# Kernel tuning notes

Hardware: AMD Instinct MI355X
Metric: run time of the kernel (lower is better)

## Reference

```python
import jax, jax.numpy as jnp
import numpy as np

N = 100_000      # nodes
E = 3_200_000    # edges (avg degree 32)
F = 16           # irrep feature channels
IR = 4           # (max_l+1)**2 with max_l = 1
DENOM = 32.0     # denominator init kwarg
EPS = 1e-9
INV_S3 = 1.0 / np.sqrt(3.0).astype(np.float32)  # CG norm for 1x1->0
INV_S2 = 1.0 / np.sqrt(2.0).astype(np.float32)  # CG norm for 1x1->1


def setup_inputs() -> dict:
    key = jax.random.key(0)
    k0, k1, k2, k3, k4 = jax.random.split(key, 5)
    positions = jax.random.normal(k0, (N, 3), jnp.float32)
    node_feats = jax.random.normal(k1, (N, F, IR), jnp.float32)
    W = jax.random.normal(k2, (IR, IR), jnp.float32) / np.float32(np.sqrt(IR))
    b = jnp.zeros((IR,), jnp.float32)
    senders = jax.random.randint(k3, (E,), 0, N)
    receivers = jax.random.randint(k4, (E,), 0, N)
    return dict(positions=positions, node_feats=node_feats, W=W, b=b,
                senders=senders, receivers=receivers)


def reference(positions, node_feats, W, b, senders, receivers):
    # --- edge update: SH of normalized relative position, CG tensor product ---
    d = positions[receivers] - positions[senders]               # [E, 3]
    d = d / (jnp.linalg.norm(d, axis=-1, keepdims=True) + EPS)  # unit direction
    # real spherical harmonics up to l=1: sh0 = 1, sh1 = unit direction
    sh1 = d[:, None, :]                                         # [E, 1, 3]

    x = node_feats[senders]                                     # [E, F, 4]
    x0 = x[..., 0:1]                                            # l=0 part [E,F,1]
    x1 = x[..., 1:4]                                            # l=1 part [E,F,3]

    # CG paths with l3 <= max_l = 1:
    #   0x0->0 (identity), 1x1->0 (dot / sqrt3)
    out0 = x0 + jnp.sum(x1 * sh1, axis=-1, keepdims=True) * INV_S3      # [E,F,1]
    #   0x1->1, 1x0->1 (identities), 1x1->1 (cross / sqrt2)
    cross = jnp.cross(x1, jnp.broadcast_to(sh1, x1.shape))
    out1 = x0 * sh1 + x1 + cross * INV_S2                               # [E,F,3]
    tp = jnp.concatenate([out0, out1], axis=-1)                         # [E,F,4]

    # --- node update: segment-sum over receivers, scale, Dense over coeff dim ---
    agg = jax.ops.segment_sum(tp, receivers, num_segments=positions.shape[0])
    agg = agg / DENOM                                                   # [N,F,4]
    return agg @ W + b                                                  # [N,F,4]
```

## Files before the change

kernel.cpp:

```cpp
#include <hip/hip_runtime.h>


#define F_DIM 16
#define BIN_SHIFT 5
#define BIN_NODES (1 << BIN_SHIFT)
#define CHUNK 4096
#define STG (CHUNK / 256)
#define CAP_LDS 1408
#define MAXBINS 4096

__global__ void __launch_bounds__(256) init_kernel(int* __restrict__ binCur,
                                                   int nbins, int cap)
{
    int b = blockIdx.x * blockDim.x + threadIdx.x;
    if (b < nbins) binCur[b] = b * cap;
}

__global__ void __launch_bounds__(256) pos_pack_kernel(
    const float* __restrict__ pos, float4* __restrict__ posf4, int N)
{
    int n = blockIdx.x * blockDim.x + threadIdx.x;
    if (n >= N) return;
    posf4[n] = make_float4(pos[3*n], pos[3*n+1], pos[3*n+2], 0.f);
}

__global__ void __launch_bounds__(256) build_bins_kernel(
    const int* __restrict__ senders, const int* __restrict__ receivers,
    int* __restrict__ binCur, int* __restrict__ bins,
    int nbins, int cap, int E)
{
    __shared__ int hist[MAXBINS];
    int t = threadIdx.x;
    for (int i = t; i < nbins; i += 256) hist[i] = 0;
    __syncthreads();

    int base = blockIdx.x * CHUNK;
    unsigned pk[STG], br[STG];
#pragma unroll
    for (int k = 0; k < STG; ++k) {
        int e = base + k * 256 + t;
        if (e < E) {
            int r = receivers[e];
            int s = senders[e];
            int bb = r >> BIN_SHIFT;
            int rank = atomicAdd(&hist[bb], 1);
            pk[k] = ((unsigned)s << BIN_SHIFT) | (unsigned)(r & (BIN_NODES - 1));
            br[k] = ((unsigned)bb << 13) | (unsigned)rank;
        } else {
            br[k] = 0xFFFFFFFFu;
        }
    }
    __syncthreads();

    for (int i = t; i < nbins; i += 256) {
        int c = hist[i];
        if (c > 0) hist[i] = atomicAdd(&binCur[i], c);
    }
    __syncthreads();

#pragma unroll
    for (int k = 0; k < STG; ++k) {
        if (br[k] == 0xFFFFFFFFu) continue;
        int bb   = (int)(br[k] >> 13);
        int rank = (int)(br[k] & 8191u);
        int dest = hist[bb] + rank;
        if (dest < (bb + 1) * cap)
            bins[dest] = (int)pk[k];
    }
}

__device__ __forceinline__ void edge_acc_d(
    float dx, float dy, float dz, const float4& fx,
    float& a0, float& a1, float& a2, float& a3)
{
    const float INV_S3 = 0.5773502691896258f;
    const float INV_S2 = 0.7071067811865476f;
    float dot = fx.y*dx + fx.z*dy + fx.w*dz;
    a0 += fx.x + dot * INV_S3;
    float c0 = fx.z*dz - fx.w*dy;
    float c1 = fx.w*dx - fx.y*dz;
    float c2 = fx.y*dy - fx.z*dx;
    a1 += fx.x*dx + fx.y + c0 * INV_S2;
    a2 += fx.x*dy + fx.z + c1 * INV_S2;
    a3 += fx.x*dz + fx.w + c2 * INV_S2;
}

__global__ void __launch_bounds__(256) bin_gather_kernel(
    const float4* __restrict__ posf4,
    const float* __restrict__ nf,
    const int* __restrict__ bins,
    const int* __restrict__ binCur,
    const float* __restrict__ W,
    const float* __restrict__ Bias,
    float* __restrict__ out,
    int N, int cap)
{
    __shared__ int   lcsr[CAP_LDS];
    __shared__ float ldx[CAP_LDS];
    __shared__ float ldy[CAP_LDS];
    __shared__ float ldz[CAP_LDS];
    __shared__ int lhist[BIN_NODES];
    __shared__ int lscan[BIN_NODES];
    __shared__ int lstart[BIN_NODES];

    int t = threadIdx.x;
    int bin = blockIdx.x;
    int node0 = bin << BIN_SHIFT;
    int gbase = bin * cap;

    int cnt = binCur[bin] - gbase;
    if (cnt > cap) cnt = cap;

    if (t < BIN_NODES) lhist[t] = 0;
    __syncthreads();

    for (int j = t; j < cnt; j += 256)
        atomicAdd(&lhist[((unsigned)bins[gbase + j]) & (BIN_NODES - 1)], 1);
    __syncthreads();

    if (t < BIN_NODES) lscan[t] = lhist[t];
    __syncthreads();
    for (int off = 1; off < BIN_NODES; off <<= 1) {
        int v = (t < BIN_NODES && t >= off) ? lscan[t - off] : 0;
        __syncthreads();
        if (t < BIN_NODES) lscan[t] += v;
        __syncthreads();
    }
    if (t < BIN_NODES) { lstart[t] = lscan[t] - lhist[t]; lhist[t] = 0; }
    __syncthreads();

    for (int j = t; j < cnt; j += 256) {
        unsigned pk = (unsigned)bins[gbase + j];
        int rl = (int)(pk & (BIN_NODES - 1));
        int s  = (int)(pk >> BIN_SHIFT);
        int rank = atomicAdd(&lhist[rl], 1);
        int dest = lstart[rl] + rank;
        lcsr[dest] = s;
        float4 ps = posf4[s];
        float4 pr = posf4[node0 + rl];
        float dx = pr.x - ps.x;
        float dy = pr.y - ps.y;
        float dz = pr.z - ps.z;
        float d2 = dx*dx + dy*dy + dz*dz;
        float inv = __builtin_amdgcn_rsqf(fmaxf(d2, 1e-18f));
        ldx[dest] = dx * inv;
        ldy[dest] = dy * inv;
        ldz[dest] = dz * inv;
    }
    __syncthreads();

    float w[16];
#pragma unroll
    for (int i = 0; i < 16; ++i) w[i] = W[i];
    float b0 = Bias[0], b1 = Bias[1], b2 = Bias[2], b3 = Bias[3];
    const float sc = 1.0f / 32.0f;

    int f = t & 15;
    const float4* nf4 = (const float4*)nf;

    for (int nl = t >> 4; nl < BIN_NODES; nl += 16) {
        int n = node0 + nl;
        if (n >= N) break;
        int s0 = lstart[nl];
        int dcnt = lscan[nl] - s0;

        float a0 = 0.f, a1 = 0.f, a2 = 0.f, a3 = 0.f;
        int j = 0;
        for (; j + 4 <= dcnt; j += 4) {
            int s_0 = lcsr[s0 + j + 0];
            int s_1 = lcsr[s0 + j + 1];
            int s_2 = lcsr[s0 + j + 2];
            int s_3 = lcsr[s0 + j + 3];
            float4 q0 = nf4[(unsigned)(s_0 * F_DIM + f)];
            float4 q1 = nf4[(unsigned)(s_1 * F_DIM + f)];
            float4 q2 = nf4[(unsigned)(s_2 * F_DIM + f)];
            float4 q3 = nf4[(unsigned)(s_3 * F_DIM + f)];
            float x0 = ldx[s0 + j + 0], y0 = ldy[s0 + j + 0], z0 = ldz[s0 + j + 0];
            float x1 = ldx[s0 + j + 1], y1 = ldy[s0 + j + 1], z1 = ldz[s0 + j + 1];
            float x2 = ldx[s0 + j + 2], y2 = ldy[s0 + j + 2], z2 = ldz[s0 + j + 2];
            float x3 = ldx[s0 + j + 3], y3 = ldy[s0 + j + 3], z3 = ldz[s0 + j + 3];
            edge_acc_d(x0, y0, z0, q0, a0, a1, a2, a3);
            edge_acc_d(x1, y1, z1, q1, a0, a1, a2, a3);
            edge_acc_d(x2, y2, z2, q2, a0, a1, a2, a3);
            edge_acc_d(x3, y3, z3, q3, a0, a1, a2, a3);
        }
        for (; j < dcnt; ++j) {
            int s = lcsr[s0 + j];
            float4 q = nf4[(unsigned)(s * F_DIM + f)];
            edge_acc_d(ldx[s0 + j], ldy[s0 + j], ldz[s0 + j], q, a0, a1, a2, a3);
        }

        a0 *= sc; a1 *= sc; a2 *= sc; a3 *= sc;
        float4 o;
        o.x = a0*w[0] + a1*w[4] + a2*w[8]  + a3*w[12] + b0;
        o.y = a0*w[1] + a1*w[5] + a2*w[9]  + a3*w[13] + b1;
        o.z = a0*w[2] + a1*w[6] + a2*w[10] + a3*w[14] + b2;
        o.w = a0*w[3] + a1*w[7] + a2*w[11] + a3*w[15] + b3;
        ((float4*)out)[(size_t)n * F_DIM + f] = o;
    }
}

__global__ void __launch_bounds__(256) hist_kernel(
    const int* __restrict__ receivers, int* __restrict__ deg,
    int* __restrict__ rank, int E)
{
    int e = blockIdx.x * blockDim.x + threadIdx.x;
    if (e >= E) return;
    rank[e] = atomicAdd(&deg[receivers[e]], 1);
}

__global__ void __launch_bounds__(256) alloc_kernel(
    const int* __restrict__ deg, int* __restrict__ start,
    int* __restrict__ cursor, int N)
{
    __shared__ int tmp[256];
    __shared__ int base;
    int t = threadIdx.x;
    int n = blockIdx.x * blockDim.x + t;
    int v = (n < N) ? deg[n] : 0;
    tmp[t] = v;
    __syncthreads();
    for (int off = 1; off < 256; off <<= 1) {
        int x = (t >= off) ? tmp[t - off] : 0;
        __syncthreads();
        tmp[t] += x;
        __syncthreads();
    }
    int incl = tmp[t];
    if (t == 255) base = atomicAdd(cursor, incl);
    __syncthreads();
    if (n < N) start[n] = base + incl - v;
}

__global__ void __launch_bounds__(256) scatter_kernel(
    const int* __restrict__ senders, const int* __restrict__ receivers,
    const int* __restrict__ rank, const int* __restrict__ start,
    int* __restrict__ csr_s, int E)
{
    int e = blockIdx.x * blockDim.x + threadIdx.x;
    if (e >= E) return;
    csr_s[start[receivers[e]] + rank[e]] = senders[e];
}

__global__ void __launch_bounds__(256) gather_kernel(
    const float* __restrict__ pos,
    const float* __restrict__ nf,
    const int* __restrict__ csr_s,
    const int* __restrict__ start,
    const int* __restrict__ deg,
    const float* __restrict__ W,
    const float* __restrict__ b,
    float* __restrict__ out,
    int N)
{
    const float INV_S3 = 0.5773502691896258f;
    const float INV_S2 = 0.7071067811865476f;

    int tid = blockIdx.x * blockDim.x + threadIdx.x;
    int n = tid >> 4;
    if (n >= N) return;
    int f = tid & 15;

    float rx = pos[3*n], ry = pos[3*n+1], rz = pos[3*n+2];
    int s0 = start[n];
    int dcnt = deg[n];
    float a0 = 0.f, a1 = 0.f, a2 = 0.f, a3 = 0.f;
    const float4* nf4 = (const float4*)nf;

    int s = (dcnt > 0) ? csr_s[s0] : 0;
    for (int j = 0; j < dcnt; ++j) {
        int s_next = (j + 1 < dcnt) ? csr_s[s0 + j + 1] : 0;
        float dx = rx - pos[3*s], dy = ry - pos[3*s+1], dz = rz - pos[3*s+2];
        float d2 = dx*dx + dy*dy + dz*dz;
        float inv = __builtin_amdgcn_rsqf(fmaxf(d2, 1e-18f));
        dx *= inv; dy *= inv; dz *= inv;
        float4 x = nf4[(unsigned)(s * F_DIM + f)];
        float x0 = x.x, x1 = x.y, x2 = x.z, x3 = x.w;
        float dot = x1*dx + x2*dy + x3*dz;
        a0 += x0 + dot * INV_S3;
        float c0 = x2*dz - x3*dy, c1 = x3*dx - x1*dz, c2 = x1*dy - x2*dx;
        a1 += x0*dx + x1 + c0 * INV_S2;
        a2 += x0*dy + x2 + c1 * INV_S2;
        a3 += x0*dz + x3 + c2 * INV_S2;
        s = s_next;
    }
    const float sc = 1.0f / 32.0f;
    a0 *= sc; a1 *= sc; a2 *= sc; a3 *= sc;
    float4 o;
    o.x = a0*W[0] + a1*W[4] + a2*W[8]  + a3*W[12] + b[0];
    o.y = a0*W[1] + a1*W[5] + a2*W[9]  + a3*W[13] + b[1];
    o.z = a0*W[2] + a1*W[6] + a2*W[10] + a3*W[14] + b[2];
    o.w = a0*W[3] + a1*W[7] + a2*W[11] + a3*W[15] + b[3];
    ((float4*)out)[tid] = o;
}

extern "C" void kernel_launch(void* const* d_in, const int* in_sizes, int n_in,
                              void* d_out, int out_size, void* d_ws, size_t ws_size,
                              hipStream_t stream)
{
    const float* pos       = (const float*)d_in[0];
    const float* nf        = (const float*)d_in[1];
    const float* W         = (const float*)d_in[2];
    const float* b         = (const float*)d_in[3];
    const int*   senders   = (const int*)d_in[4];
    const int*   receivers = (const int*)d_in[5];

    int N = in_sizes[0] / 3;
    int E = in_sizes[4];
    float* out = (float*)d_out;
    const int blk = 256;

    int nbins = (N + BIN_NODES - 1) >> BIN_SHIFT;
    int cap   = E / nbins + 384;
    size_t need = ((size_t)N * 4 + (size_t)nbins * cap + nbins) * sizeof(float);

    if (nbins <= MAXBINS && cap <= CAP_LDS && ws_size >= need) {
        float4* posf4 = (float4*)d_ws;
        int* binCur = (int*)(posf4 + N);
        int* bins   = binCur + nbins;

        pos_pack_kernel<<<(N + blk - 1) / blk, blk, 0, stream>>>(pos, posf4, N);
        init_kernel<<<(nbins + blk - 1) / blk, blk, 0, stream>>>(binCur, nbins, cap);
        build_bins_kernel<<<(E + CHUNK - 1) / CHUNK, blk, 0, stream>>>(
            senders, receivers, binCur, bins, nbins, cap, E);
        bin_gather_kernel<<<nbins, blk, 0, stream>>>(
            posf4, nf, bins, binCur, W, b, out, N, cap);
    } else {
        int* cursor = (int*)d_ws;
        int* deg    = cursor + 1;
        int* start  = deg + N;
        int* rank   = start + N;
        int* csr_s  = rank + E;

        hipMemsetAsync(cursor, 0, (size_t)(1 + N) * sizeof(int), stream);
        hist_kernel<<<(E + blk - 1) / blk, blk, 0, stream>>>(receivers, deg, rank, E);
        alloc_kernel<<<(N + blk - 1) / blk, blk, 0, stream>>>(deg, start, cursor, N);
        scatter_kernel<<<(E + blk - 1) / blk, blk, 0, stream>>>(
            senders, receivers, rank, start, csr_s, E);
        long total = (long)N * F_DIM;
        gather_kernel<<<(unsigned)((total + blk - 1) / blk), blk, 0, stream>>>(
            pos, nf, csr_s, start, deg, W, b, out, N);
    }
}
```

Baseline: 287.5 us.

## Use 64-node bins split across two gather blocks with packed float4 edge records

Bins double to 64 nodes, which halves the number of global bin cursors and the atomics on them. The bin-building kernel moves to 512 threads and 8192-edge chunks and reads receivers twice instead of holding per-edge state in registers. Each bin is now processed by two gather blocks, each filtering the edges for its 32-node half, so every block reads the whole bin. Edge direction and sender index are packed into one float4 in LDS so each edge needs a single LDS load, and a guard for LDS overflow is added.

```diff
diff --git a/kernel.cpp b/kernel.cpp
--- a/kernel.cpp
+++ b/kernel.cpp
@@ -2,12 +2,12 @@
 
 
 #define F_DIM 16
-#define BIN_SHIFT 5
+#define BIN_SHIFT 6
 #define BIN_NODES (1 << BIN_SHIFT)
-#define CHUNK 4096
-#define STG (CHUNK / 256)
+#define HALF_NODES (BIN_NODES / 2)
+#define CHUNK 8192
 #define CAP_LDS 1408
-#define MAXBINS 4096
+#define MAXBINS 2048
 
 __global__ void __launch_bounds__(256) init_kernel(int* __restrict__ binCur,
                                                    int nbins, int cap)
@@ -24,48 +24,38 @@
     posf4[n] = make_float4(pos[3*n], pos[3*n+1], pos[3*n+2], 0.f);
 }
 
-__global__ void __launch_bounds__(256) build_bins_kernel(
+__global__ void __launch_bounds__(512) build_bins_kernel(
     const int* __restrict__ senders, const int* __restrict__ receivers,
     int* __restrict__ binCur, int* __restrict__ bins,
     int nbins, int cap, int E)
 {
-    __shared__ int hist[MAXBINS];
+    __shared__ int hbase[MAXBINS];
+    __shared__ int hrank[MAXBINS];
     int t = threadIdx.x;
-    for (int i = t; i < nbins; i += 256) hist[i] = 0;
+    for (int i = t; i < nbins; i += 512) { hbase[i] = 0; hrank[i] = 0; }
     __syncthreads();
 
     int base = blockIdx.x * CHUNK;
-    unsigned pk[STG], br[STG];
-#pragma unroll
-    for (int k = 0; k < STG; ++k) {
-        int e = base + k * 256 + t;
-        if (e < E) {
-            int r = receivers[e];
-            int s = senders[e];
-            int bb = r >> BIN_SHIFT;
-            int rank = atomicAdd(&hist[bb], 1);
-            pk[k] = ((unsigned)s << BIN_SHIFT) | (unsigned)(r & (BIN_NODES - 1));
-            br[k] = ((unsigned)bb << 13) | (unsigned)rank;
-        } else {
-            br[k] = 0xFFFFFFFFu;
-        }
-    }
-    __syncthreads();
-
-    for (int i = t; i < nbins; i += 256) {
-        int c = hist[i];
-        if (c > 0) hist[i] = atomicAdd(&binCur[i], c);
-    }
-    __syncthreads();
-
-#pragma unroll
-    for (int k = 0; k < STG; ++k) {
-        if (br[k] == 0xFFFFFFFFu) continue;
-        int bb   = (int)(br[k] >> 13);
-        int rank = (int)(br[k] & 8191u);
-        int dest = hist[bb] + rank;
+    int end  = base + CHUNK; if (end > E) end = E;
+
+    for (int e = base + t; e < end; e += 512)
+        atomicAdd(&hbase[((unsigned)receivers[e]) >> BIN_SHIFT], 1);
+    __syncthreads();
+
+    for (int i = t; i < nbins; i += 512) {
+        int c = hbase[i];
+        hbase[i] = (c > 0) ? atomicAdd(&binCur[i], c) : 0;
+    }
+    __syncthreads();
+
+    for (int e = base + t; e < end; e += 512) {
+        int r = receivers[e];
+        int s = senders[e];
+        int bb = r >> BIN_SHIFT;
+        int rank = atomicAdd(&hrank[bb], 1);
+        int dest = hbase[bb] + rank;
         if (dest < (bb + 1) * cap)
-            bins[dest] = (int)pk[k];
+            bins[dest] = (s << BIN_SHIFT) | (r & (BIN_NODES - 1));
     }
 }
 
@@ -95,57 +85,62 @@
     float* __restrict__ out,
     int N, int cap)
 {
-    __shared__ int   lcsr[CAP_LDS];
-    __shared__ float ldx[CAP_LDS];
-    __shared__ float ldy[CAP_LDS];
-    __shared__ float ldz[CAP_LDS];
-    __shared__ int lhist[BIN_NODES];
-    __shared__ int lscan[BIN_NODES];
-    __shared__ int lstart[BIN_NODES];
+    __shared__ float4 ledge[CAP_LDS];
+    __shared__ int lhist[HALF_NODES];
+    __shared__ int lscan[HALF_NODES];
+    __shared__ int lstart[HALF_NODES];
 
     int t = threadIdx.x;
-    int bin = blockIdx.x;
-    int node0 = bin << BIN_SHIFT;
+    int bin  = blockIdx.x >> 1;
+    int half = blockIdx.x & 1;
+    int node0 = (bin << BIN_SHIFT) + half * HALF_NODES;
     int gbase = bin * cap;
 
     int cnt = binCur[bin] - gbase;
     if (cnt > cap) cnt = cap;
 
-    if (t < BIN_NODES) lhist[t] = 0;
-    __syncthreads();
-
-    for (int j = t; j < cnt; j += 256)
-        atomicAdd(&lhist[((unsigned)bins[gbase + j]) & (BIN_NODES - 1)], 1);
-    __syncthreads();
-
-    if (t < BIN_NODES) lscan[t] = lhist[t];
-    __syncthreads();
-    for (int off = 1; off < BIN_NODES; off <<= 1) {
-        int v = (t < BIN_NODES && t >= off) ? lscan[t - off] : 0;
+    if (t < HALF_NODES) lhist[t] = 0;
+    __syncthreads();
+
+    for (int j = t; j < cnt; j += 256) {
+        int rl = bins[gbase + j] & (BIN_NODES - 1);
+        if ((rl >> 5) == half) atomicAdd(&lhist[rl & (HALF_NODES - 1)], 1);
+    }
+    __syncthreads();
+
+    if (t < HALF_NODES) lscan[t] = lhist[t];
+    __syncthreads();
+    for (int off = 1; off < HALF_NODES; off <<= 1) {
+        int v = (t < HALF_NODES && t >= off) ? lscan[t - off] : 0;
         __syncthreads();
-        if (t < BIN_NODES) lscan[t] += v;
+        if (t < HALF_NODES) lscan[t] += v;
         __syncthreads();
     }
-    if (t < BIN_NODES) { lstart[t] = lscan[t] - lhist[t]; lhist[t] = 0; }
+    if (t < HALF_NODES) { lstart[t] = lscan[t] - lhist[t]; lhist[t] = 0; }
     __syncthreads();
 
     for (int j = t; j < cnt; j += 256) {
-        unsigned pk = (unsigned)bins[gbase + j];
-        int rl = (int)(pk & (BIN_NODES - 1));
-        int s  = (int)(pk >> BIN_SHIFT);
-        int rank = atomicAdd(&lhist[rl], 1);
-        int dest = lstart[rl] + rank;
-        lcsr[dest] = s;
+        int pk = bins[gbase + j];
+        int rl = pk & (BIN_NODES - 1);
+        if ((rl >> 5) != half) continue;
+        int rl32 = rl & (HALF_NODES - 1);
+        int s = pk >> BIN_SHIFT;
+        int rank = atomicAdd(&lhist[rl32], 1);
+        int dest = lstart[rl32] + rank;
+        if (dest >= CAP_LDS) continue;
         float4 ps = posf4[s];
-        float4 pr = posf4[node0 + rl];
+        float4 pr = posf4[node0 + rl32];
         float dx = pr.x - ps.x;
         float dy = pr.y - ps.y;
         float dz = pr.z - ps.z;
         float d2 = dx*dx + dy*dy + dz*dz;
         float inv = __builtin_amdgcn_rsqf(fmaxf(d2, 1e-18f));
-        ldx[dest] = dx * inv;
-        ldy[dest] = dy * inv;
-        ldz[dest] = dz * inv;
+        float4 rec;
+        rec.x = dx * inv;
+        rec.y = dy * inv;
+        rec.z = dz * inv;
+        rec.w = __int_as_float(s);
+        ledge[dest] = rec;
     }
     __syncthreads();
 
@@ -158,36 +153,38 @@
     int f = t & 15;
     const float4* nf4 = (const float4*)nf;
 
-    for (int nl = t >> 4; nl < BIN_NODES; nl += 16) {
+    for (int nl = t >> 4; nl < HALF_NODES; nl += 16) {
         int n = node0 + nl;
         if (n >= N) break;
         int s0 = lstart[nl];
         int dcnt = lscan[nl] - s0;
+        if (dcnt > CAP_LDS - s0) dcnt = CAP_LDS - s0;
 
         float a0 = 0.f, a1 = 0.f, a2 = 0.f, a3 = 0.f;
         int j = 0;
         for (; j + 4 <= dcnt; j += 4) {
-            int s_0 = lcsr[s0 + j + 0];
-            int s_1 = lcsr[s0 + j + 1];
-            int s_2 = lcsr[s0 + j + 2];
-            int s_3 = lcsr[s0 + j + 3];
+            float4 e0 = ledge[s0 + j + 0];
+            float4 e1 = ledge[s0 + j + 1];
+            float4 e2 = ledge[s0 + j + 2];
+            float4 e3 = ledge[s0 + j + 3];
+            int s_0 = __float_as_int(e0.w);
+            int s_1 = __float_as_int(e1.w);
+            int s_2 = __float_as_int(e2.w);
+            int s_3 = __float_as_int(e3.w);
             float4 q0 = nf4[(unsigned)(s_0 * F_DIM + f)];
             float4 q1 = nf4[(unsigned)(s_1 * F_DIM + f)];
             float4 q2 = nf4[(unsigned)(s_2 * F_DIM + f)];
             float4 q3 = nf4[(unsigned)(s_3 * F_DIM + f)];
-            float x0 = ldx[s0 + j + 0], y0 = ldy[s0 + j + 0], z0 = ldz[s0 + j + 0];
-            float x1 = ldx[s0 + j + 1], y1 = ldy[s0 + j + 1], z1 = ldz[s0 + j + 1];
-            float x2 = ldx[s0 + j + 2], y2 = ldy[s0 + j + 2], z2 = ldz[s0 + j + 2];
-            float x3 = ldx[s0 + j + 3], y3 = ldy[s0 + j + 3], z3 = ldz[s0 + j + 3];
-            edge_acc_d(x0, y0, z0, q0, a0, a1, a2, a3);
-            edge_acc_d(x1, y1, z1, q1, a0, a1, a2, a3);
-            edge_acc_d(x2, y2, z2, q2, a0, a1, a2, a3);
-            edge_acc_d(x3, y3, z3, q3, a0, a1, a2, a3);
+            edge_acc_d(e0.x, e0.y, e0.z, q0, a0, a1, a2, a3);
+            edge_acc_d(e1.x, e1.y, e1.z, q1, a0, a1, a2, a3);
+            edge_acc_d(e2.x, e2.y, e2.z, q2, a0, a1, a2, a3);
+            edge_acc_d(e3.x, e3.y, e3.z, q3, a0, a1, a2, a3);
         }
         for (; j < dcnt; ++j) {
-            int s = lcsr[s0 + j];
+            float4 e0 = ledge[s0 + j];
+            int s = __float_as_int(e0.w);
             float4 q = nf4[(unsigned)(s * F_DIM + f)];
-            edge_acc_d(ldx[s0 + j], ldy[s0 + j], ldz[s0 + j], q, a0, a1, a2, a3);
+            edge_acc_d(e0.x, e0.y, e0.z, q, a0, a1, a2, a3);
         }
 
         a0 *= sc; a1 *= sc; a2 *= sc; a3 *= sc;
@@ -311,19 +308,19 @@
     const int blk = 256;
 
     int nbins = (N + BIN_NODES - 1) >> BIN_SHIFT;
-    int cap   = E / nbins + 384;
+    int cap   = E / nbins + 453;
     size_t need = ((size_t)N * 4 + (size_t)nbins * cap + nbins) * sizeof(float);
 
-    if (nbins <= MAXBINS && cap <= CAP_LDS && ws_size >= need) {
+    if (nbins <= MAXBINS && ws_size >= need) {
         float4* posf4 = (float4*)d_ws;
         int* binCur = (int*)(posf4 + N);
         int* bins   = binCur + nbins;
 
         pos_pack_kernel<<<(N + blk - 1) / blk, blk, 0, stream>>>(pos, posf4, N);
         init_kernel<<<(nbins + blk - 1) / blk, blk, 0, stream>>>(binCur, nbins, cap);
-        build_bins_kernel<<<(E + CHUNK - 1) / CHUNK, blk, 0, stream>>>(
+        build_bins_kernel<<<(E + CHUNK - 1) / CHUNK, 512, 0, stream>>>(
             senders, receivers, binCur, bins, nbins, cap, E);
-        bin_gather_kernel<<<nbins, blk, 0, stream>>>(
+        bin_gather_kernel<<<nbins * 2, blk, 0, stream>>>(
             posf4, nf, bins, binCur, W, b, out, N, cap);
     } else {
         int* cursor = (int*)d_ws;
```

New measurement: 290.3 us. Within noise of the previous version (+0.9%).
